# Optimization experiments

Measured on AMD Instinct MI355X. Metric: run time of the kernel, lower is better.

Reference implementation:

```python
import jax, jax.numpy as jnp
import numpy as np

L = 8          # context_length
P = 196        # patches_per_frame
PT = 16        # patches_per_tactile_frame
N_EMBD = 768
N_HEAD = 12
BATCH = 4
T = (L + 1) + L * PT + L * P  # 1705


def build_mask(L, P, Pt):
    # image-query block rows (L*P rows)
    mi = np.zeros((L * P, L * P))
    a1 = np.zeros((L * P, L + 1))
    t1 = np.zeros((L * P, L * Pt))
    for i in range(L):
        mi[i * P:(i + 1) * P, :(i + 1) * P] = 1
        a1[i * P:(i + 2) * P, :i + 2] = 1
        t1[i * P:(i + 1) * P, :(i + 1) * Pt] = 1
    m1 = np.concatenate([a1, t1, mi], axis=1)
    # tactile-query block rows (L*Pt rows)
    a2 = np.zeros((L * Pt, L + 1))
    t2 = np.zeros((L * Pt, L * Pt))
    i2 = np.zeros((L * Pt, L * P))
    for i in range(L):
        a2[i * Pt:(i + 2) * Pt, :i + 2] = 1
        t2[i * Pt:(i + 1) * Pt, :(i + 1) * Pt] = 1
        i2[i * Pt:(i + 1) * Pt, :(i + 1) * P] = 1
    m2 = np.concatenate([a2, t2, i2], axis=1)
    # action-query rows (L+1 rows)
    a3 = np.zeros((L + 1, L + 1))
    t3 = np.zeros((L + 1, L * Pt))
    i3 = np.zeros((L + 1, L * P))
    for i in range(L + 1):
        a3[i:i + 2, :i + 2] = 1
        t3[i:i + 1, :(i + 1) * Pt] = 1
        i3[i:i + 1, :(i + 1) * P] = 1
    m3 = np.concatenate([a3, t3, i3], axis=1)
    return np.concatenate([m3, m2, m1], axis=0).astype(bool)


def setup_inputs() -> dict:
    key = jax.random.key(0)
    k1, k2, k3 = jax.random.split(key, 3)
    x = jax.random.normal(k1, (BATCH, T, N_EMBD), dtype=jnp.float32)
    W_attn = jax.random.normal(k2, (N_EMBD, 3 * N_EMBD), dtype=jnp.float32) * 0.02
    W_proj = jax.random.normal(k3, (N_EMBD, N_EMBD), dtype=jnp.float32) * 0.02
    mask = jnp.asarray(build_mask(L, P, PT))
    return {"x": x, "W_attn": W_attn, "W_proj": W_proj, "mask": mask, "n_head": N_HEAD}


def reference(x, W_attn, W_proj, mask, n_head):
    B, Tq, C = x.shape
    hd = C // n_head
    qkv = x @ W_attn                      # [B, T, 3C]
    q, k, v = jnp.split(qkv, 3, axis=-1)
    # [B, H, T, hd]
    q = q.reshape(B, Tq, n_head, hd).transpose(0, 2, 1, 3)
    k = k.reshape(B, Tq, n_head, hd).transpose(0, 2, 1, 3)
    v = v.reshape(B, Tq, n_head, hd).transpose(0, 2, 1, 3)
    scores = jnp.einsum("bhqd,bhkd->bhqk", q, k) / jnp.sqrt(jnp.float32(hd))
    scores = jnp.where(mask[None, None, :, :], scores, jnp.float32(-1e9))
    probs = jax.nn.softmax(scores, axis=-1)
    y = jnp.einsum("bhqk,bhkd->bhqd", probs, v)
    y = y.transpose(0, 2, 1, 3).reshape(B, Tq, C)
    return y @ W_proj
```

## Files before the change

### kernel.cpp

```cpp
#include <hip/hip_runtime.h>
#include <hip/hip_bf16.h>

typedef __attribute__((ext_vector_type(8))) short short8;
typedef __attribute__((ext_vector_type(4))) float f32x4;

#define MFMA16(a,b,c) __builtin_amdgcn_mfma_f32_16x16x32_bf16((a),(b),(c),0,0,0)

#define WAITVM(N) asm volatile("s_waitcnt vmcnt(" #N ")" ::: "memory")
#define BAR()     asm volatile("s_barrier" ::: "memory")

constexpr int Tt = 1705;
constexpr int Tp = 1792;
constexpr int NKT_ALL = 28;
constexpr int NH = 12, HD = 64, Bb = 4, C_ = 768;
constexpr int M_  = Bb * Tt;
constexpr int Mp  = 6912;
constexpr int NQT = 14;
constexpr int NCH = 4;
constexpr float QSCALE = 0.18033688011116016f;

static_assert(Mp % 256 == 0 && (3 * C_) % 256 == 0, "256-tile grid");

__device__ __forceinline__ void gl16(const void* g, void* l) {
  __builtin_amdgcn_global_load_lds((const __attribute__((address_space(1))) void*)g,
                                   (__attribute__((address_space(3))) void*)l, 16, 0, 0);
}

__device__ __forceinline__ float ex2(float x) {
  float r; asm("v_exp_f32 %0, %1" : "=v"(r) : "v"(x)); return r;
}

__device__ __forceinline__ int frame_of(int t) {
  return t < 9 ? t : (t < 137 ? ((t - 9) >> 4) : ((t - 137) / 196));
}

__device__ __forceinline__ int lim16(int a) {
  if (a >= Tt) return 0;
  int bnd = min(a + 15, Tt - 1);
  int fmax = (a == 0) ? 8 : frame_of(min(bnd, a < 137 ? 136 : bnd));
  return (fmax >= 8) ? Tt : 137 + (fmax + 1) * 196;
}

__global__ __launch_bounds__(256) void k_conv_x(const float* __restrict__ x,
                                                __hip_bfloat16* __restrict__ xb) {
  int i = blockIdx.x * 256 + threadIdx.x;
  if (i >= Mp * C_ / 4) return;
  float4 v = make_float4(0.f, 0.f, 0.f, 0.f);
  if (i * 4 < M_ * C_) v = ((const float4*)x)[i];
  __hip_bfloat16 o0 = __float2bfloat16(v.x), o1 = __float2bfloat16(v.y),
                 o2 = __float2bfloat16(v.z), o3 = __float2bfloat16(v.w);
  ushort4 u = make_ushort4(*(unsigned short*)&o0, *(unsigned short*)&o1,
                           *(unsigned short*)&o2, *(unsigned short*)&o3);
  ((ushort4*)xb)[i] = u;
}

__global__ __launch_bounds__(256) void k_transpose_w(const float* __restrict__ src,
                                                     __hip_bfloat16* __restrict__ dst,
                                                     int K, int N) {
  __shared__ float tile[32][33];
  int kb = blockIdx.x * 32, nb = blockIdx.y * 32;
  int tx = threadIdx.x & 31, ty = threadIdx.x >> 5;
  for (int i = 0; i < 4; i++)
    tile[ty + i * 8][tx] = src[(size_t)(kb + ty + i * 8) * N + nb + tx];
  __syncthreads();
  for (int i = 0; i < 4; i++)
    dst[(size_t)(nb + ty + i * 8) * K + kb + tx] = __float2bfloat16(tile[tx][ty + i * 8]);
}

__global__ __launch_bounds__(512) void k_gemm_qkv(const __hip_bfloat16* __restrict__ xb,
                                                  const __hip_bfloat16* __restrict__ wat,
                                                  __hip_bfloat16* __restrict__ q,
                                                  __hip_bfloat16* __restrict__ kpk,
                                                  __hip_bfloat16* __restrict__ vpk) {
  __shared__ __hip_bfloat16 As[4][256 * 32], Bs[4][256 * 32];
  const int tid = threadIdx.x;
  const int lane = tid & 63, w = tid >> 6;
  const int wr = w >> 2, wc = w & 3;
  const int l16 = lane & 15, grp = lane >> 4;
  const int m0 = blockIdx.x * 256, n0 = blockIdx.y * 256;
  constexpr int NT = C_ / 32;

  auto stage = [&](int t, int bb) {
    int k0 = t * 32;
    for (int p = 0; p < 2; p++) {
      int idx = p * 512 + tid;
      int row = idx >> 2;
      int c8 = (idx & 3) ^ ((row >> 1) & 3);
      gl16(xb  + (size_t)(m0 + row) * C_ + k0 + c8 * 8, &As[bb][idx * 8]);
      gl16(wat + (size_t)(n0 + row) * C_ + k0 + c8 * 8, &Bs[bb][idx * 8]);
    }
  };

  f32x4 acc[8][4];
  for (int i = 0; i < 8; i++)
    for (int j = 0; j < 4; j++) { f32x4 z = {0.f,0.f,0.f,0.f}; acc[i][j] = z; }

  stage(0, 0); stage(1, 1); stage(2, 2);

  for (int t = 0; t < NT; t++) {
    if (t + 3 < NT) stage(t + 3, (t + 3) & 3);
    int rem = NT - 1 - t;
    if (rem >= 3)      WAITVM(12);
    else if (rem == 2) WAITVM(8);
    else if (rem == 1) WAITVM(4);
    else               WAITVM(0);
    BAR();
    const __hip_bfloat16* Ac = As[t & 3];
    const __hip_bfloat16* Bc = Bs[t & 3];
    short8 bfr[4], afr[4];
    for (int nj = 0; nj < 4; nj++) {
      int row = wc * 64 + nj * 16 + l16;
      bfr[nj] = *(const short8*)(Bc + row * 32 + ((grp ^ ((row >> 1) & 3)) * 8));
    }
    for (int mi = 0; mi < 4; mi++) {
      int row = wr * 128 + mi * 16 + l16;
      afr[mi] = *(const short8*)(Ac + row * 32 + ((grp ^ ((row >> 1) & 3)) * 8));
    }
    __builtin_amdgcn_s_setprio(1);
    for (int mi = 0; mi < 4; mi++)
      for (int nj = 0; nj < 4; nj++)
        acc[mi][nj] = MFMA16(afr[mi], bfr[nj], acc[mi][nj]);
    __builtin_amdgcn_s_setprio(0);
    for (int mi = 0; mi < 4; mi++) {
      int row = wr * 128 + 64 + mi * 16 + l16;
      afr[mi] = *(const short8*)(Ac + row * 32 + ((grp ^ ((row >> 1) & 3)) * 8));
    }
    __builtin_amdgcn_s_setprio(1);
    for (int mi = 0; mi < 4; mi++)
      for (int nj = 0; nj < 4; nj++)
        acc[4 + mi][nj] = MFMA16(afr[mi], bfr[nj], acc[4 + mi][nj]);
    __builtin_amdgcn_s_setprio(0);
    BAR();
  }

  const int which = n0 / C_;
  const int c0 = n0 - which * C_ + wc * 64;
  for (int mi = 0; mi < 8; mi++)
    for (int r = 0; r < 4; r++) {
      int m = m0 + wr * 128 + mi * 16 + grp * 4 + r;
      if (m >= M_) continue;
      int b = m / Tt, t = m - b * Tt;
      for (int nj = 0; nj < 4; nj++) {
        int c = c0 + nj * 16 + l16;
        int h = c >> 6, d = c & 63;
        float val = acc[mi][nj][r];
        int bh = b * NH + h;
        if (which == 0) {
          q[((size_t)bh * Tp + t) * HD + d] = __float2bfloat16(val * QSCALE);
        } else if (which == 1) {
          int kt = t >> 6, jj = (t >> 4) & 3, mm = t & 15;
          int half = d >> 5, gg = (d >> 3) & 3, ss = d & 7;
          kpk[(((size_t)bh * NKT_ALL + kt) * 8 + jj * 2 + half) * 512 +
              (gg * 16 + mm) * 8 + ss] = __float2bfloat16(val);
        } else {
          int kt = t >> 6, kb2 = (t >> 5) & 1, k32 = t & 31;
          int gg = (k32 >> 2) & 3, ss = (k32 & 3) + ((k32 >> 4) & 1) * 4;
          int jt = d >> 4, mm = d & 15;
          vpk[(((size_t)bh * NKT_ALL + kt) * 8 + jt * 2 + kb2) * 512 +
              (gg * 16 + mm) * 8 + ss] = __float2bfloat16(val);
        }
      }
    }
}

__global__ __launch_bounds__(256) void k_gemm_proj64(const __hip_bfloat16* __restrict__ A,
                                                     const __hip_bfloat16* __restrict__ Bt,
                                                     float* __restrict__ out) {
  __shared__ __hip_bfloat16 As[4][64 * 32], Bs[4][128 * 32];
  const int tid = threadIdx.x;
  const int lane = tid & 63, w = tid >> 6;
  const int l16 = lane & 15, grp = lane >> 4;
  const int m0 = blockIdx.x * 64, n0 = blockIdx.y * 128;
  f32x4 acc[8];
  for (int j = 0; j < 8; j++) { f32x4 z = {0.f,0.f,0.f,0.f}; acc[j] = z; }

  auto stage = [&](int t, int bb) {
    int k0 = t * 32;
    int row = tid >> 2;
    int c8 = (tid & 3) ^ ((row >> 1) & 3);
    gl16(A + (size_t)(m0 + row) * C_ + k0 + c8 * 8, &As[bb][tid * 8]);
    for (int rr = 0; rr < 2; rr++) {
      int idx = rr * 256 + tid;
      int brow = idx >> 2;
      int bc8 = (idx & 3) ^ ((brow >> 1) & 3);
      gl16(Bt + (size_t)(n0 + brow) * C_ + k0 + bc8 * 8, &Bs[bb][idx * 8]);
    }
  };

  constexpr int NT = C_ / 32;
  stage(0, 0); stage(1, 1); stage(2, 2);

  for (int t = 0; t < NT; t++) {
    if (t + 3 < NT) stage(t + 3, (t + 3) & 3);
    int rem = NT - 1 - t;
    if (rem >= 3)      WAITVM(9);
    else if (rem == 2) WAITVM(6);
    else if (rem == 1) WAITVM(3);
    else               WAITVM(0);
    BAR();
    const __hip_bfloat16* Ac = As[t & 3];
    const __hip_bfloat16* Bc = Bs[t & 3];
    int arow = w * 16 + l16;
    short8 a = *(const short8*)(Ac + arow * 32 + ((grp ^ ((arow >> 1) & 3)) * 8));
    __builtin_amdgcn_s_setprio(1);
    for (int j = 0; j < 8; j++) {
      int brow = j * 16 + l16;
      short8 b = *(const short8*)(Bc + brow * 32 + ((grp ^ ((brow >> 1) & 3)) * 8));
      acc[j] = MFMA16(a, b, acc[j]);
    }
    __builtin_amdgcn_s_setprio(0);
    BAR();
  }

  for (int r = 0; r < 4; r++) {
    int m = m0 + w * 16 + grp * 4 + r;
    if (m >= M_) continue;
    for (int j = 0; j < 8; j++)
      out[(size_t)m * C_ + n0 + j * 16 + l16] = acc[j][r];
  }
}

union S8u { short8 v; struct { unsigned long long lo, hi; } q; unsigned u[4]; };

__device__ __forceinline__ unsigned pack2bf(float a, float b) {
  union { __hip_bfloat162 h; unsigned u; } cv;
  cv.h = __float22bfloat162_rn(make_float2(a, b));
  return cv.u;
}

__global__ __launch_bounds__(256, 2) void k_attn(const __hip_bfloat16* __restrict__ q,
                                                 const __hip_bfloat16* __restrict__ kpk,
                                                 const __hip_bfloat16* __restrict__ vpk,
                                                 __hip_bfloat16* __restrict__ Opart,
                                                 float* __restrict__ lpart) {
  const int tid = threadIdx.x, lane = tid & 63, w = tid >> 6;
  const int l16 = lane & 15, grp = lane >> 4;
  const int id = blockIdx.x;
  const int xslot = id & 7, rr_ = id >> 3;
  const int bh = xslot + 8 * (rr_ / 56);
  const int cq = rr_ % 56;
  const int qt = cq >> 2, ch = cq & (NCH - 1);
  const int t0q = qt * 128;
  const __hip_bfloat16* qb = q + (size_t)bh * Tp * HD;

  int lim[2], Cmn[2], Ath[2], Bth[2], Cth[2];
  for (int g = 0; g < 2; g++) {
    int a = t0q + w * 32 + g * 16;
    lim[g] = lim16(a);
    int fqmn, fql;
    if (a >= Tt) { fqmn = 8; fql = 8; }
    else {
      int bnd = min(a + 15, Tt - 1);
      fqmn = min(frame_of(a), frame_of(bnd));
      int t = a + l16;
      fql = (t >= Tt) ? 8 : frame_of(t);
    }
    Cmn[g] = min(137 + 196 * (fqmn + 1), Tt);
    Ath[g] = fql + 2;
    Bth[g] = 9 + 16 * (fql + 1);
    Cth[g] = min(137 + 196 * (fql + 1), Tt);
  }
  int limw = max(lim[0], lim[1]);
  int nktw = (limw + 63) >> 6;
  int k0t = (ch * nktw) >> 2;
  int k1t = ((ch + 1) * nktw) >> 2;

  short8 qa[2][2];
  for (int g = 0; g < 2; g++) {
    const __hip_bfloat16* qr = qb + (size_t)(t0q + w * 32 + g * 16 + l16) * HD + grp * 8;
    qa[g][0] = *(const short8*)(qr);
    qa[g][1] = *(const short8*)(qr + 32);
  }
  f32x4 o[2][4];
  for (int g = 0; g < 2; g++)
    for (int jt = 0; jt < 4; jt++) { f32x4 z = {0.f,0.f,0.f,0.f}; o[g][jt] = z; }
  f32x4 ps[2];
  { f32x4 z = {0.f,0.f,0.f,0.f}; ps[0] = z; ps[1] = z; }

  const short8* kbase = (const short8*)(kpk + (size_t)bh * NKT_ALL * 4096);
  const short8* vbase = (const short8*)(vpk + (size_t)bh * NKT_ALL * 4096);

  for (int kt = k0t; kt < k1t; kt++) {
    const int t0k = kt * 64;
    const short8* kp = kbase + (size_t)kt * 512;
    const short8* vp = vbase + (size_t)kt * 512;
    short8 kf[4][2], vf[4][2];
    for (int j = 0; j < 4; j++)
      for (int hh = 0; hh < 2; hh++) kf[j][hh] = kp[(j * 2 + hh) * 64 + lane];
    for (int jt = 0; jt < 4; jt++)
      for (int kb2 = 0; kb2 < 2; kb2++) vf[jt][kb2] = vp[(jt * 2 + kb2) * 64 + lane];

    f32x4 s[2][4];
    for (int j = 0; j < 4; j++) {
      f32x4 z = {0.f,0.f,0.f,0.f};
      s[0][j] = MFMA16(kf[j][0], qa[0][0], z);
      s[0][j] = MFMA16(kf[j][1], qa[0][1], s[0][j]);
      s[1][j] = MFMA16(kf[j][0], qa[1][0], z);
      s[1][j] = MFMA16(kf[j][1], qa[1][1], s[1][j]);
    }

    bool act0 = t0k < lim[0], act1 = t0k < lim[1];
    bool fullk = (t0k + 64 <= Tt);
    S8u pf[2][2];
    for (int g = 0; g < 2; g++) {
      bool act = g == 0 ? act0 : act1;
      if (!act) continue;
      bool needm = !(fullk && (t0k >= 192 ? (t0k + 64) <= Cmn[g] : Cmn[g] >= Tt));
      if (needm) {
        for (int j = 0; j < 4; j++)
          for (int r = 0; r < 4; r++) {
            int key = t0k + j * 16 + grp * 4 + r;
            int thr = key < 9 ? Ath[g] : (key < 137 ? Bth[g] : Cth[g]);
            if (key >= thr) s[g][j][r] = -1e30f;
          }
      }
      f32x4 p[4];
      for (int j = 0; j < 4; j++)
        for (int r = 0; r < 4; r++) p[j][r] = ex2(s[g][j][r]);
      ps[g] += (p[0] + p[1]) + (p[2] + p[3]);
      pf[g][0].u[0] = pack2bf(p[0][0], p[0][1]);
      pf[g][0].u[1] = pack2bf(p[0][2], p[0][3]);
      pf[g][0].u[2] = pack2bf(p[1][0], p[1][1]);
      pf[g][0].u[3] = pack2bf(p[1][2], p[1][3]);
      pf[g][1].u[0] = pack2bf(p[2][0], p[2][1]);
      pf[g][1].u[1] = pack2bf(p[2][2], p[2][3]);
      pf[g][1].u[2] = pack2bf(p[3][0], p[3][1]);
      pf[g][1].u[3] = pack2bf(p[3][2], p[3][3]);
    }

    for (int jt = 0; jt < 4; jt++)
      for (int kb2 = 0; kb2 < 2; kb2++) {
        if (act0) o[0][jt] = MFMA16(vf[jt][kb2], pf[0][kb2].v, o[0][jt]);
        if (act1) o[1][jt] = MFMA16(vf[jt][kb2], pf[1][kb2].v, o[1][jt]);
      }
  }

  float lr[2];
  for (int g = 0; g < 2; g++) {
    float sum = (ps[g][0] + ps[g][1]) + (ps[g][2] + ps[g][3]);
    sum += __shfl_xor(sum, 16);
    sum += __shfl_xor(sum, 32);
    lr[g] = sum;
  }

  const int blk = bh * (NQT * NCH) + cq;
  __hip_bfloat16* op = Opart + (size_t)blk * (128 * 64);
  for (int g = 0; g < 2; g++) {
    int row = w * 32 + g * 16 + l16;
    for (int jt = 0; jt < 4; jt++) {
      unsigned p01 = pack2bf(o[g][jt][0], o[g][jt][1]);
      unsigned p23 = pack2bf(o[g][jt][2], o[g][jt][3]);
      ushort4 u;
      u.x = p01 & 0xffff; u.y = p01 >> 16; u.z = p23 & 0xffff; u.w = p23 >> 16;
      *(ushort4*)(op + row * 64 + jt * 16 + grp * 4) = u;
    }
    if (grp == 0) lpart[(size_t)blk * 128 + w * 32 + g * 16 + l16] = lr[g];
  }
}

__global__ __launch_bounds__(256) void k_combine(const __hip_bfloat16* __restrict__ Opart,
                                                 const float* __restrict__ lpart,
                                                 __hip_bfloat16* __restrict__ y) {
  const int tid = threadIdx.x;
  const int qt = blockIdx.x, bh = blockIdx.y;
  const int b = bh / NH, h = bh - b * NH;
  const int t0q = qt * 128;
  const int blk0 = bh * (NQT * NCH) + qt * NCH;
  __shared__ float ls[128];
  if (tid < 128) {
    float s = 0.f;
    for (int c = 0; c < NCH; c++) s += lpart[(size_t)(blk0 + c) * 128 + tid];
    ls[tid] = (s > 0.f) ? 1.0f / s : 0.f;
  }
  __syncthreads();
  for (int it = 0; it < 4; it++) {
    int e8 = it * 256 + tid;
    int e = e8 * 8;
    int row = e >> 6, d = e & 63;
    int t = t0q + row;
    if (t >= Tt) continue;
    float acc[8] = {0,0,0,0,0,0,0,0};
    for (int c = 0; c < NCH; c++) {
      short8 vv = *(const short8*)(Opart + (size_t)(blk0 + c) * (128 * 64) + e);
      for (int i = 0; i < 8; i++) {
        union { unsigned u; float f; } cv;
        cv.u = ((unsigned)(unsigned short)vv[i]) << 16;
        acc[i] += cv.f;
      }
    }
    float rinv = ls[row];
    short8 outv;
    for (int i = 0; i < 8; i += 2) {
      unsigned p = pack2bf(acc[i] * rinv, acc[i + 1] * rinv);
      outv[i] = (short)(p & 0xffff);
      outv[i + 1] = (short)(p >> 16);
    }
    *(short8*)(y + (size_t)(b * Tt + t) * C_ + h * 64 + d) = outv;
  }
}

extern "C" void kernel_launch(void* const* d_in, const int* in_sizes, int n_in,
                              void* d_out, int out_size, void* d_ws, size_t ws_size,
                              hipStream_t stream) {
  const float* x  = (const float*)d_in[0];
  const float* Wa = (const float*)d_in[1];
  const float* Wp = (const float*)d_in[2];
  float* out = (float*)d_out;

  char* ws = (char*)d_ws;
  size_t off = 0;
  auto alloc = [&](size_t bytes) { size_t r = off; off += (bytes + 255) & ~(size_t)255; return r; };
  __hip_bfloat16* xb  = (__hip_bfloat16*)(ws + alloc((size_t)Mp * C_ * 2));
  __hip_bfloat16* wat = (__hip_bfloat16*)(ws + alloc((size_t)3 * C_ * C_ * 2));
  __hip_bfloat16* wpt = (__hip_bfloat16*)(ws + alloc((size_t)C_ * C_ * 2));
  __hip_bfloat16* qb  = (__hip_bfloat16*)(ws + alloc((size_t)Bb * NH * Tp * HD * 2));
  __hip_bfloat16* kpk = (__hip_bfloat16*)(ws + alloc((size_t)Bb * NH * NKT_ALL * 4096 * 2));
  __hip_bfloat16* vpk = (__hip_bfloat16*)(ws + alloc((size_t)Bb * NH * NKT_ALL * 4096 * 2));
  __hip_bfloat16* yb  = (__hip_bfloat16*)(ws + alloc((size_t)Mp * C_ * 2));
  __hip_bfloat16* Opart = (__hip_bfloat16*)(ws + alloc((size_t)Bb * NH * NQT * NCH * 128 * 64 * 2));
  float*          lpart = (float*)(ws + alloc((size_t)Bb * NH * NQT * NCH * 128 * 4));

  k_conv_x<<<(Mp * C_ / 4 + 255) / 256, 256, 0, stream>>>(x, xb);
  k_transpose_w<<<dim3(C_ / 32, 3 * C_ / 32), 256, 0, stream>>>(Wa, wat, C_, 3 * C_);
  k_transpose_w<<<dim3(C_ / 32, C_ / 32), 256, 0, stream>>>(Wp, wpt, C_, C_);
  k_gemm_qkv<<<dim3(Mp / 256, 3 * C_ / 256), 512, 0, stream>>>(xb, wat, qb, kpk, vpk);
  k_attn<<<dim3(Bb * NH * NQT * NCH), 256, 0, stream>>>(qb, kpk, vpk, Opart, lpart);
  k_combine<<<dim3(NQT, Bb * NH), 256, 0, stream>>>(Opart, lpart, yb);
  k_gemm_proj64<<<dim3(Mp / 64, C_ / 128), 256, 0, stream>>>(yb, wpt, out);
}
```

Baseline: 221.3 us.

## Remap attention waves to share query rows, double-buffer KV loads, raise MFMA priority

```diff
diff --git a/kernel.cpp b/kernel.cpp
--- a/kernel.cpp
+++ b/kernel.cpp
@@ -239,13 +239,15 @@
   const int xslot = id & 7, rr_ = id >> 3;
   const int bh = xslot + 8 * (rr_ / 56);
   const int cq = rr_ % 56;
-  const int qt = cq >> 2, ch = cq & (NCH - 1);
+  const int qt = cq >> 2, wslot = cq & 3;
+  const int ch = w;
   const int t0q = qt * 128;
+  const int a0 = t0q + wslot * 32;
   const __hip_bfloat16* qb = q + (size_t)bh * Tp * HD;
 
   int lim[2], Cmn[2], Ath[2], Bth[2], Cth[2];
   for (int g = 0; g < 2; g++) {
-    int a = t0q + w * 32 + g * 16;
+    int a = a0 + g * 16;
     lim[g] = lim16(a);
     int fqmn, fql;
     if (a >= Tt) { fqmn = 8; fql = 8; }
@@ -267,7 +269,7 @@
 
   short8 qa[2][2];
   for (int g = 0; g < 2; g++) {
-    const __hip_bfloat16* qr = qb + (size_t)(t0q + w * 32 + g * 16 + l16) * HD + grp * 8;
+    const __hip_bfloat16* qr = qb + (size_t)(a0 + g * 16 + l16) * HD + grp * 8;
     qa[g][0] = *(const short8*)(qr);
     qa[g][1] = *(const short8*)(qr + 32);
   }
@@ -280,17 +282,19 @@
   const short8* kbase = (const short8*)(kpk + (size_t)bh * NKT_ALL * 4096);
   const short8* vbase = (const short8*)(vpk + (size_t)bh * NKT_ALL * 4096);
 
-  for (int kt = k0t; kt < k1t; kt++) {
-    const int t0k = kt * 64;
+  auto loadKV = [&](int kt, short8 (&kf)[4][2], short8 (&vf)[4][2]) {
     const short8* kp = kbase + (size_t)kt * 512;
     const short8* vp = vbase + (size_t)kt * 512;
-    short8 kf[4][2], vf[4][2];
     for (int j = 0; j < 4; j++)
       for (int hh = 0; hh < 2; hh++) kf[j][hh] = kp[(j * 2 + hh) * 64 + lane];
     for (int jt = 0; jt < 4; jt++)
       for (int kb2 = 0; kb2 < 2; kb2++) vf[jt][kb2] = vp[(jt * 2 + kb2) * 64 + lane];
-
+  };
+
+  auto do_tile = [&](int kt, const short8 (&kf)[4][2], const short8 (&vf)[4][2]) {
+    const int t0k = kt * 64;
     f32x4 s[2][4];
+    __builtin_amdgcn_s_setprio(1);
     for (int j = 0; j < 4; j++) {
       f32x4 z = {0.f,0.f,0.f,0.f};
       s[0][j] = MFMA16(kf[j][0], qa[0][0], z);
@@ -298,6 +302,7 @@
       s[1][j] = MFMA16(kf[j][0], qa[1][0], z);
       s[1][j] = MFMA16(kf[j][1], qa[1][1], s[1][j]);
     }
+    __builtin_amdgcn_s_setprio(0);
 
     bool act0 = t0k < lim[0], act1 = t0k < lim[1];
     bool fullk = (t0k + 64 <= Tt);
@@ -328,11 +333,29 @@
       pf[g][1].u[3] = pack2bf(p[3][2], p[3][3]);
     }
 
+    __builtin_amdgcn_s_setprio(1);
     for (int jt = 0; jt < 4; jt++)
       for (int kb2 = 0; kb2 < 2; kb2++) {
         if (act0) o[0][jt] = MFMA16(vf[jt][kb2], pf[0][kb2].v, o[0][jt]);
         if (act1) o[1][jt] = MFMA16(vf[jt][kb2], pf[1][kb2].v, o[1][jt]);
       }
+    __builtin_amdgcn_s_setprio(0);
+  };
+
+  short8 kfA[4][2], vfA[4][2], kfB[4][2], vfB[4][2];
+  int kt = k0t;
+  if (kt < k1t) {
+    loadKV(kt, kfA, vfA);
+    for (;;) {
+      if (kt + 1 < k1t) loadKV(kt + 1, kfB, vfB);
+      do_tile(kt, kfA, vfA);
+      kt++;
+      if (kt >= k1t) break;
+      if (kt + 1 < k1t) loadKV(kt + 1, kfA, vfA);
+      do_tile(kt, kfB, vfB);
+      kt++;
+      if (kt >= k1t) break;
+    }
   }
 
   float lr[2];
@@ -343,10 +366,10 @@
     lr[g] = sum;
   }
 
-  const int blk = bh * (NQT * NCH) + cq;
+  const int blk = bh * (NQT * NCH) + qt * NCH + ch;
   __hip_bfloat16* op = Opart + (size_t)blk * (128 * 64);
   for (int g = 0; g < 2; g++) {
-    int row = w * 32 + g * 16 + l16;
+    int row = wslot * 32 + g * 16 + l16;
     for (int jt = 0; jt < 4; jt++) {
       unsigned p01 = pack2bf(o[g][jt][0], o[g][jt][1]);
       unsigned p23 = pack2bf(o[g][jt][2], o[g][jt][3]);
@@ -354,7 +377,7 @@
       u.x = p01 & 0xffff; u.y = p01 >> 16; u.z = p23 & 0xffff; u.w = p23 >> 16;
       *(ushort4*)(op + row * 64 + jt * 16 + grp * 4) = u;
     }
-    if (grp == 0) lpart[(size_t)blk * 128 + w * 32 + g * 16 + l16] = lr[g];
+    if (grp == 0) lpart[(size_t)blk * 128 + row] = lr[g];
   }
 }
 
```

Result: slower. 232.8 us (+5.2%).

## Restructure attention split: each wave handles 64 query rows over half the keys

Applied to the files above, without the earlier changes.

```diff
diff --git a/kernel.cpp b/kernel.cpp
--- a/kernel.cpp
+++ b/kernel.cpp
@@ -16,7 +16,7 @@
 constexpr int M_  = Bb * Tt;
 constexpr int Mp  = 6912;
 constexpr int NQT = 14;
-constexpr int NCH = 4;
+constexpr int NCHA = 2;
 constexpr float QSCALE = 0.18033688011116016f;
 
 static_assert(Mp % 256 == 0 && (3 * C_) % 256 == 0, "256-tile grid");
@@ -235,17 +235,19 @@
                                                  float* __restrict__ lpart) {
   const int tid = threadIdx.x, lane = tid & 63, w = tid >> 6;
   const int l16 = lane & 15, grp = lane >> 4;
+  const int rp = w >> 1, ch = w & 1;
   const int id = blockIdx.x;
   const int xslot = id & 7, rr_ = id >> 3;
-  const int bh = xslot + 8 * (rr_ / 56);
-  const int cq = rr_ % 56;
-  const int qt = cq >> 2, ch = cq & (NCH - 1);
+  const int oct = rr_ / NQT;
+  const int bh = xslot + 8 * oct;
+  const int qt = rr_ - oct * NQT;
   const int t0q = qt * 128;
+  const int a0 = t0q + rp * 64;
   const __hip_bfloat16* qb = q + (size_t)bh * Tp * HD;
 
-  int lim[2], Cmn[2], Ath[2], Bth[2], Cth[2];
-  for (int g = 0; g < 2; g++) {
-    int a = t0q + w * 32 + g * 16;
+  int lim[4], Cmn[4], Ath[4], Bth[4], Cth[4];
+  for (int g = 0; g < 4; g++) {
+    int a = a0 + g * 16;
     lim[g] = lim16(a);
     int fqmn, fql;
     if (a >= Tt) { fqmn = 8; fql = 8; }
@@ -260,22 +262,22 @@
     Bth[g] = 9 + 16 * (fql + 1);
     Cth[g] = min(137 + 196 * (fql + 1), Tt);
   }
-  int limw = max(lim[0], lim[1]);
+  int limw = max(max(lim[0], lim[1]), max(lim[2], lim[3]));
   int nktw = (limw + 63) >> 6;
-  int k0t = (ch * nktw) >> 2;
-  int k1t = ((ch + 1) * nktw) >> 2;
-
-  short8 qa[2][2];
-  for (int g = 0; g < 2; g++) {
-    const __hip_bfloat16* qr = qb + (size_t)(t0q + w * 32 + g * 16 + l16) * HD + grp * 8;
+  int k0t = (ch * nktw) >> 1;
+  int k1t = ((ch + 1) * nktw) >> 1;
+
+  short8 qa[4][2];
+  for (int g = 0; g < 4; g++) {
+    const __hip_bfloat16* qr = qb + (size_t)(a0 + g * 16 + l16) * HD + grp * 8;
     qa[g][0] = *(const short8*)(qr);
     qa[g][1] = *(const short8*)(qr + 32);
   }
-  f32x4 o[2][4];
-  for (int g = 0; g < 2; g++)
+  f32x4 o[4][4];
+  for (int g = 0; g < 4; g++)
     for (int jt = 0; jt < 4; jt++) { f32x4 z = {0.f,0.f,0.f,0.f}; o[g][jt] = z; }
-  f32x4 ps[2];
-  { f32x4 z = {0.f,0.f,0.f,0.f}; ps[0] = z; ps[1] = z; }
+  f32x4 ps[4];
+  for (int g = 0; g < 4; g++) { f32x4 z = {0.f,0.f,0.f,0.f}; ps[g] = z; }
 
   const short8* kbase = (const short8*)(kpk + (size_t)bh * NKT_ALL * 4096);
   const short8* vbase = (const short8*)(vpk + (size_t)bh * NKT_ALL * 4096);
@@ -290,63 +292,59 @@
     for (int jt = 0; jt < 4; jt++)
       for (int kb2 = 0; kb2 < 2; kb2++) vf[jt][kb2] = vp[(jt * 2 + kb2) * 64 + lane];
 
-    f32x4 s[2][4];
-    for (int j = 0; j < 4; j++) {
-      f32x4 z = {0.f,0.f,0.f,0.f};
-      s[0][j] = MFMA16(kf[j][0], qa[0][0], z);
-      s[0][j] = MFMA16(kf[j][1], qa[0][1], s[0][j]);
-      s[1][j] = MFMA16(kf[j][0], qa[1][0], z);
-      s[1][j] = MFMA16(kf[j][1], qa[1][1], s[1][j]);
-    }
-
-    bool act0 = t0k < lim[0], act1 = t0k < lim[1];
-    bool fullk = (t0k + 64 <= Tt);
-    S8u pf[2][2];
-    for (int g = 0; g < 2; g++) {
-      bool act = g == 0 ? act0 : act1;
-      if (!act) continue;
+    const bool fullk = (t0k + 64 <= Tt);
+    for (int g = 0; g < 4; g++) {
+      if (t0k >= lim[g]) continue;
+      f32x4 s[4];
+      __builtin_amdgcn_s_setprio(1);
+      for (int j = 0; j < 4; j++) {
+        f32x4 z = {0.f,0.f,0.f,0.f};
+        s[j] = MFMA16(kf[j][0], qa[g][0], z);
+        s[j] = MFMA16(kf[j][1], qa[g][1], s[j]);
+      }
+      __builtin_amdgcn_s_setprio(0);
       bool needm = !(fullk && (t0k >= 192 ? (t0k + 64) <= Cmn[g] : Cmn[g] >= Tt));
       if (needm) {
         for (int j = 0; j < 4; j++)
           for (int r = 0; r < 4; r++) {
             int key = t0k + j * 16 + grp * 4 + r;
             int thr = key < 9 ? Ath[g] : (key < 137 ? Bth[g] : Cth[g]);
-            if (key >= thr) s[g][j][r] = -1e30f;
+            if (key >= thr) s[j][r] = -1e30f;
           }
       }
       f32x4 p[4];
       for (int j = 0; j < 4; j++)
-        for (int r = 0; r < 4; r++) p[j][r] = ex2(s[g][j][r]);
+        for (int r = 0; r < 4; r++) p[j][r] = ex2(s[j][r]);
       ps[g] += (p[0] + p[1]) + (p[2] + p[3]);
-      pf[g][0].u[0] = pack2bf(p[0][0], p[0][1]);
-      pf[g][0].u[1] = pack2bf(p[0][2], p[0][3]);
-      pf[g][0].u[2] = pack2bf(p[1][0], p[1][1]);
-      pf[g][0].u[3] = pack2bf(p[1][2], p[1][3]);
-      pf[g][1].u[0] = pack2bf(p[2][0], p[2][1]);
-      pf[g][1].u[1] = pack2bf(p[2][2], p[2][3]);
-      pf[g][1].u[2] = pack2bf(p[3][0], p[3][1]);
-      pf[g][1].u[3] = pack2bf(p[3][2], p[3][3]);
-    }
-
-    for (int jt = 0; jt < 4; jt++)
-      for (int kb2 = 0; kb2 < 2; kb2++) {
-        if (act0) o[0][jt] = MFMA16(vf[jt][kb2], pf[0][kb2].v, o[0][jt]);
-        if (act1) o[1][jt] = MFMA16(vf[jt][kb2], pf[1][kb2].v, o[1][jt]);
-      }
-  }
-
-  float lr[2];
-  for (int g = 0; g < 2; g++) {
+      S8u pf[2];
+      pf[0].u[0] = pack2bf(p[0][0], p[0][1]);
+      pf[0].u[1] = pack2bf(p[0][2], p[0][3]);
+      pf[0].u[2] = pack2bf(p[1][0], p[1][1]);
+      pf[0].u[3] = pack2bf(p[1][2], p[1][3]);
+      pf[1].u[0] = pack2bf(p[2][0], p[2][1]);
+      pf[1].u[1] = pack2bf(p[2][2], p[2][3]);
+      pf[1].u[2] = pack2bf(p[3][0], p[3][1]);
+      pf[1].u[3] = pack2bf(p[3][2], p[3][3]);
+      __builtin_amdgcn_s_setprio(1);
+      for (int jt = 0; jt < 4; jt++)
+        for (int kb2 = 0; kb2 < 2; kb2++)
+          o[g][jt] = MFMA16(vf[jt][kb2], pf[kb2].v, o[g][jt]);
+      __builtin_amdgcn_s_setprio(0);
+    }
+  }
+
+  float lr[4];
+  for (int g = 0; g < 4; g++) {
     float sum = (ps[g][0] + ps[g][1]) + (ps[g][2] + ps[g][3]);
     sum += __shfl_xor(sum, 16);
     sum += __shfl_xor(sum, 32);
     lr[g] = sum;
   }
 
-  const int blk = bh * (NQT * NCH) + cq;
+  const int blk = bh * (NQT * NCHA) + qt * NCHA + ch;
   __hip_bfloat16* op = Opart + (size_t)blk * (128 * 64);
-  for (int g = 0; g < 2; g++) {
-    int row = w * 32 + g * 16 + l16;
+  for (int g = 0; g < 4; g++) {
+    int row = rp * 64 + g * 16 + l16;
     for (int jt = 0; jt < 4; jt++) {
       unsigned p01 = pack2bf(o[g][jt][0], o[g][jt][1]);
       unsigned p23 = pack2bf(o[g][jt][2], o[g][jt][3]);
@@ -354,7 +352,7 @@
       u.x = p01 & 0xffff; u.y = p01 >> 16; u.z = p23 & 0xffff; u.w = p23 >> 16;
       *(ushort4*)(op + row * 64 + jt * 16 + grp * 4) = u;
     }
-    if (grp == 0) lpart[(size_t)blk * 128 + w * 32 + g * 16 + l16] = lr[g];
+    if (grp == 0) lpart[(size_t)blk * 128 + row] = lr[g];
   }
 }
 
@@ -365,11 +363,11 @@
   const int qt = blockIdx.x, bh = blockIdx.y;
   const int b = bh / NH, h = bh - b * NH;
   const int t0q = qt * 128;
-  const int blk0 = bh * (NQT * NCH) + qt * NCH;
+  const int blk0 = bh * (NQT * NCHA) + qt * NCHA;
   __shared__ float ls[128];
   if (tid < 128) {
     float s = 0.f;
-    for (int c = 0; c < NCH; c++) s += lpart[(size_t)(blk0 + c) * 128 + tid];
+    for (int c = 0; c < NCHA; c++) s += lpart[(size_t)(blk0 + c) * 128 + tid];
     ls[tid] = (s > 0.f) ? 1.0f / s : 0.f;
   }
   __syncthreads();
@@ -380,7 +378,7 @@
     int t = t0q + row;
     if (t >= Tt) continue;
     float acc[8] = {0,0,0,0,0,0,0,0};
-    for (int c = 0; c < NCH; c++) {
+    for (int c = 0; c < NCHA; c++) {
       short8 vv = *(const short8*)(Opart + (size_t)(blk0 + c) * (128 * 64) + e);
       for (int i = 0; i < 8; i++) {
         union { unsigned u; float f; } cv;
@@ -417,14 +415,14 @@
   __hip_bfloat16* kpk = (__hip_bfloat16*)(ws + alloc((size_t)Bb * NH * NKT_ALL * 4096 * 2));
   __hip_bfloat16* vpk = (__hip_bfloat16*)(ws + alloc((size_t)Bb * NH * NKT_ALL * 4096 * 2));
   __hip_bfloat16* yb  = (__hip_bfloat16*)(ws + alloc((size_t)Mp * C_ * 2));
-  __hip_bfloat16* Opart = (__hip_bfloat16*)(ws + alloc((size_t)Bb * NH * NQT * NCH * 128 * 64 * 2));
-  float*          lpart = (float*)(ws + alloc((size_t)Bb * NH * NQT * NCH * 128 * 4));
+  __hip_bfloat16* Opart = (__hip_bfloat16*)(ws + alloc((size_t)Bb * NH * NQT * NCHA * 128 * 64 * 2));
+  float*          lpart = (float*)(ws + alloc((size_t)Bb * NH * NQT * NCHA * 128 * 4));
 
   k_conv_x<<<(Mp * C_ / 4 + 255) / 256, 256, 0, stream>>>(x, xb);
   k_transpose_w<<<dim3(C_ / 32, 3 * C_ / 32), 256, 0, stream>>>(Wa, wat, C_, 3 * C_);
   k_transpose_w<<<dim3(C_ / 32, C_ / 32), 256, 0, stream>>>(Wp, wpt, C_, C_);
   k_gemm_qkv<<<dim3(Mp / 256, 3 * C_ / 256), 512, 0, stream>>>(xb, wat, qb, kpk, vpk);
-  k_attn<<<dim3(Bb * NH * NQT * NCH), 256, 0, stream>>>(qb, kpk, vpk, Opart, lpart);
+  k_attn<<<dim3(Bb * NH * NQT), 256, 0, stream>>>(qb, kpk, vpk, Opart, lpart);
   k_combine<<<dim3(NQT, Bb * NH), 256, 0, stream>>>(Opart, lpart, yb);
   k_gemm_proj64<<<dim3(Mp / 64, C_ / 128), 256, 0, stream>>>(yb, wpt, out);
 }
```

After: 221.9 us. No clear change (+0.3%).
